# Kernel optimization log

Measured on AMD Instinct MI355X. Metric: run time of the kernel, lower is better.

The kernel has to match this reference:

```python
import jax, jax.numpy as jnp
import numpy as np

T, B, I, H = 2048, 64, 256, 256

def setup_inputs() -> dict:
    key = jax.random.key(0)
    k_x, k_wih, k_whh = jax.random.split(key, 3)
    x = jax.random.normal(k_x, (T, B, I), dtype=jnp.float32)
    h0 = jnp.zeros((1, B, H), dtype=jnp.float32)
    # nn.RNN weight_ih_l0 init: U(-1/sqrt(H), 1/sqrt(H)); shape [H, I]
    bound = 1.0 / np.sqrt(H)
    W_ih = jax.random.uniform(k_wih, (H, I), minval=-bound, maxval=bound, dtype=jnp.float32)
    # IndRNN recurrent weight: diagonal vector, U(-1, 1); biases are zeroed.
    w_hh = jax.random.uniform(k_whh, (H,), minval=-1.0, maxval=1.0, dtype=jnp.float32)
    return {"x": x, "h0": h0, "W_ih": W_ih, "w_hh": w_hh}

def reference(x, h0, W_ih, w_hh):
    # Precompute the input projection for all timesteps (the only GEMM):
    # [T, B, H] = x @ W_ih^T  (biases are zero)
    xW = jnp.einsum('tbi,hi->tbh', x, W_ih)

    def step(h, xw_t):
        # IndRNN: diagonal recurrence -> elementwise multiply instead of matmul
        h_new = jax.nn.relu(xw_t + h * w_hh)
        return h_new, h_new

    h_last, outputs = jax.lax.scan(step, h0[0], xW)
    return outputs, h_last[None]  # ([T,B,H], [1,B,H]) matching nn.RNN
```

## Files before the change

### kernel.cpp

```cpp
#include <hip/hip_runtime.h>

typedef short v8s __attribute__((ext_vector_type(8)));
typedef float v4f __attribute__((ext_vector_type(4)));

#define BATCH 16
#define NBATCH 128
#define BH 16384
#define TBH 33554432

__device__ __forceinline__ ushort f2bf(float f) {
  uint u = __float_as_uint(f);
  u += 0x7FFF + ((u >> 16) & 1);
  return (ushort)(u >> 16);
}

__device__ __forceinline__ uint pkbf2(float a, float b) {
  uint r;
  asm("v_cvt_pk_bf16_f32 %0, %1, %2" : "=v"(r) : "v"(a), "v"(b));
  return r;
}

union frag_u { uint u[4]; v8s s; };

__global__ __launch_bounds__(256, 2) void indrnn_gemm(
    const float* __restrict__ A,
    const float* __restrict__ W,
    ushort* __restrict__ C)
{
  const int tid  = threadIdx.x;
  const int lane = tid & 63;
  const int wv   = tid >> 6;
  const int l15  = lane & 15;
  const int lhi  = lane >> 4;
  const int c0   = wv * 64;
  const int rowblk = blockIdx.x * 256;

  frag_u wfr[4][8];
  #pragma unroll
  for (int nt = 0; nt < 4; ++nt) {
    const float* pw = W + (((size_t)(c0 + nt * 16 + l15)) << 8) + (lhi << 3);
    #pragma unroll
    for (int kk = 0; kk < 8; ++kk) {
      const float4 w0 = *(const float4*)(pw + kk * 32);
      const float4 w1 = *(const float4*)(pw + kk * 32 + 4);
      wfr[nt][kk].u[0] = pkbf2(w0.x, w0.y);
      wfr[nt][kk].u[1] = pkbf2(w0.z, w0.w);
      wfr[nt][kk].u[2] = pkbf2(w1.x, w1.y);
      wfr[nt][kk].u[3] = pkbf2(w1.z, w1.w);
    }
  }

  const float* pA = A + (((size_t)(rowblk + l15)) << 8) + (lhi << 3);

  float4 fa[8], fb[8];
  #pragma unroll
  for (int kk = 0; kk < 4; ++kk) {
    fa[2*kk]   = *(const float4*)(pA + kk * 32);
    fa[2*kk+1] = *(const float4*)(pA + kk * 32 + 4);
    fb[2*kk]   = *(const float4*)(pA + 128 + kk * 32);
    fb[2*kk+1] = *(const float4*)(pA + 128 + kk * 32 + 4);
  }

  for (int c = 0; c < 16; ++c) {
    v4f acc[4] = {};
    const float* pAn = pA + (size_t)(c + 1) * 4096;

    #pragma unroll
    for (int kk = 0; kk < 4; ++kk) {
      frag_u af;
      af.u[0] = pkbf2(fa[2*kk].x,   fa[2*kk].y);
      af.u[1] = pkbf2(fa[2*kk].z,   fa[2*kk].w);
      af.u[2] = pkbf2(fa[2*kk+1].x, fa[2*kk+1].y);
      af.u[3] = pkbf2(fa[2*kk+1].z, fa[2*kk+1].w);
      #pragma unroll
      for (int nt = 0; nt < 4; ++nt)
        acc[nt] = __builtin_amdgcn_mfma_f32_16x16x32_bf16(af.s, wfr[nt][kk].s, acc[nt], 0, 0, 0);
    }
    if (c + 1 < 16) {
      #pragma unroll
      for (int kk = 0; kk < 4; ++kk) {
        fa[2*kk]   = *(const float4*)(pAn + kk * 32);
        fa[2*kk+1] = *(const float4*)(pAn + kk * 32 + 4);
      }
    }

    #pragma unroll
    for (int kk = 0; kk < 4; ++kk) {
      frag_u af;
      af.u[0] = pkbf2(fb[2*kk].x,   fb[2*kk].y);
      af.u[1] = pkbf2(fb[2*kk].z,   fb[2*kk].w);
      af.u[2] = pkbf2(fb[2*kk+1].x, fb[2*kk+1].y);
      af.u[3] = pkbf2(fb[2*kk+1].z, fb[2*kk+1].w);
      #pragma unroll
      for (int nt = 0; nt < 4; ++nt)
        acc[nt] = __builtin_amdgcn_mfma_f32_16x16x32_bf16(af.s, wfr[nt][kk + 4].s, acc[nt], 0, 0, 0);
    }
    if (c + 1 < 16) {
      #pragma unroll
      for (int kk = 0; kk < 4; ++kk) {
        fb[2*kk]   = *(const float4*)(pAn + 128 + kk * 32);
        fb[2*kk+1] = *(const float4*)(pAn + 128 + kk * 32 + 4);
      }
    }

    const int mrow = rowblk + c * 16 + lhi * 4;
    #pragma unroll
    for (int nt = 0; nt < 4; ++nt) {
      const int col = c0 + nt * 16 + l15;
      #pragma unroll
      for (int r = 0; r < 4; ++r)
        C[(((size_t)(mrow + r)) << 8) + col] = f2bf(acc[nt][r]);
    }
  }
}

__global__ __launch_bounds__(64) void indrnn_scan(
    const ushort* __restrict__ xw,
    const float* __restrict__ h0,
    const float* __restrict__ w_hh,
    float* __restrict__ out)
{
  const int ch = blockIdx.x * 64 + threadIdx.x;
  const float w = w_hh[ch & 255];
  float h = h0[ch];
  const ushort* px = xw + ch;
  float* po = out + ch;

  uint b0[BATCH], b1[BATCH], b2[BATCH], b3[BATCH];

  auto ld = [&](uint (&buf)[BATCH], int kb) {
    const ushort* p = px + (size_t)kb * BATCH * BH;
    #pragma unroll
    for (int j = 0; j < BATCH; ++j) buf[j] = p[(size_t)j * BH];
  };
  auto cp = [&](uint (&buf)[BATCH], int kb) {
    float* o = po + (size_t)kb * BATCH * BH;
    #pragma unroll
    for (int j = 0; j < BATCH; ++j) {
      float xv = __uint_as_float(buf[j] << 16);
      h = fmaxf(fmaf(h, w, xv), 0.0f);
      o[(size_t)j * BH] = h;
    }
  };

  ld(b0, 0); ld(b1, 1); ld(b2, 2); ld(b3, 3);
  for (int kb = 0; kb < NBATCH; kb += 4) {
    cp(b0, kb);     if (kb + 4 < NBATCH) ld(b0, kb + 4);
    cp(b1, kb + 1); if (kb + 5 < NBATCH) ld(b1, kb + 5);
    cp(b2, kb + 2); if (kb + 6 < NBATCH) ld(b2, kb + 6);
    cp(b3, kb + 3); if (kb + 7 < NBATCH) ld(b3, kb + 7);
  }
  out[(size_t)TBH + ch] = h;
}

extern "C" void kernel_launch(void* const* d_in, const int* in_sizes, int n_in,
                              void* d_out, int out_size, void* d_ws, size_t ws_size,
                              hipStream_t stream) {
  const float* x    = (const float*)d_in[0];
  const float* h0   = (const float*)d_in[1];
  const float* W_ih = (const float*)d_in[2];
  const float* w_hh = (const float*)d_in[3];
  float* out = (float*)d_out;
  ushort* xw = (ushort*)d_ws;

  indrnn_gemm<<<dim3(512), dim3(256), 0, stream>>>(x, W_ih, xw);
  indrnn_scan<<<dim3(256), dim3(64), 0, stream>>>(xw, h0, w_hh, out);
}
```

Before: 321.1 us.

## Stage GEMM A tiles in LDS with async global_load_lds double buffering

In the input-projection GEMM, each wave used to load its own copy of the activation rows into registers. Now each 16-row A tile is loaded once per block, straight into a double-buffered, XOR-swizzled shared-memory buffer with global_load_lds, and every wave reads its fragments from LDS. The next tile's load overlaps the current tile's MFMAs, blocks are halved to 128 rows, the grid doubles and launch bounds ask for 4 blocks per CU. In exchange it adds 32 KB of LDS per block and a __syncthreads per tile, and the wait for the async loads to land relies on the barrier placement.

```diff
diff --git a/kernel.cpp b/kernel.cpp
--- a/kernel.cpp
+++ b/kernel.cpp
@@ -22,18 +22,30 @@
 
 union frag_u { uint u[4]; v8s s; };
 
-__global__ __launch_bounds__(256, 2) void indrnn_gemm(
+__global__ __launch_bounds__(256, 4) void indrnn_gemm(
     const float* __restrict__ A,
     const float* __restrict__ W,
     ushort* __restrict__ C)
 {
+  __shared__ __align__(16) float sbuf[2][4096];
+
   const int tid  = threadIdx.x;
   const int lane = tid & 63;
   const int wv   = tid >> 6;
   const int l15  = lane & 15;
   const int lhi  = lane >> 4;
   const int c0   = wv * 64;
-  const int rowblk = blockIdx.x * 256;
+  const int m0   = blockIdx.x * 128;
+
+  {
+    const float* base = A + ((size_t)m0 << 8);
+    #pragma unroll
+    for (int j = 0; j < 4; ++j) {
+      const int row = wv * 4 + j;
+      const float* src = base + (row << 8) + ((lane ^ (row & 7)) << 2);
+      __builtin_amdgcn_global_load_lds(src, &sbuf[0][row << 8], 16, 0, 0);
+    }
+  }
 
   frag_u wfr[4][8];
   #pragma unroll
@@ -50,60 +62,43 @@
     }
   }
 
-  const float* pA = A + (((size_t)(rowblk + l15)) << 8) + (lhi << 3);
+  const int swm  = (l15 & 7) << 4;
+  const int off0 = (l15 << 10) + ((lhi * 32)      ^ swm);
+  const int off1 = (l15 << 10) + ((lhi * 32 + 16) ^ swm);
 
-  float4 fa[8], fb[8];
-  #pragma unroll
-  for (int kk = 0; kk < 4; ++kk) {
-    fa[2*kk]   = *(const float4*)(pA + kk * 32);
-    fa[2*kk+1] = *(const float4*)(pA + kk * 32 + 4);
-    fb[2*kk]   = *(const float4*)(pA + 128 + kk * 32);
-    fb[2*kk+1] = *(const float4*)(pA + 128 + kk * 32 + 4);
-  }
+  __syncthreads();
 
-  for (int c = 0; c < 16; ++c) {
+  for (int c = 0; c < 8; ++c) {
+    const int cur = c & 1;
+
+    if (c + 1 < 8) {
+      const float* base = A + (((size_t)(m0 + (c + 1) * 16)) << 8);
+      #pragma unroll
+      for (int j = 0; j < 4; ++j) {
+        const int row = wv * 4 + j;
+        const float* src = base + (row << 8) + ((lane ^ (row & 7)) << 2);
+        __builtin_amdgcn_global_load_lds(src, &sbuf[cur ^ 1][row << 8], 16, 0, 0);
+      }
+    }
+
+    const char* p0 = (const char*)sbuf[cur] + off0;
+    const char* p1 = (const char*)sbuf[cur] + off1;
     v4f acc[4] = {};
-    const float* pAn = pA + (size_t)(c + 1) * 4096;
-
     #pragma unroll
-    for (int kk = 0; kk < 4; ++kk) {
+    for (int kk = 0; kk < 8; ++kk) {
+      const float4 f0 = *(const float4*)(p0 + kk * 128);
+      const float4 f1 = *(const float4*)(p1 + kk * 128);
       frag_u af;
-      af.u[0] = pkbf2(fa[2*kk].x,   fa[2*kk].y);
-      af.u[1] = pkbf2(fa[2*kk].z,   fa[2*kk].w);
-      af.u[2] = pkbf2(fa[2*kk+1].x, fa[2*kk+1].y);
-      af.u[3] = pkbf2(fa[2*kk+1].z, fa[2*kk+1].w);
+      af.u[0] = pkbf2(f0.x, f0.y);
+      af.u[1] = pkbf2(f0.z, f0.w);
+      af.u[2] = pkbf2(f1.x, f1.y);
+      af.u[3] = pkbf2(f1.z, f1.w);
       #pragma unroll
       for (int nt = 0; nt < 4; ++nt)
         acc[nt] = __builtin_amdgcn_mfma_f32_16x16x32_bf16(af.s, wfr[nt][kk].s, acc[nt], 0, 0, 0);
     }
-    if (c + 1 < 16) {
-      #pragma unroll
-      for (int kk = 0; kk < 4; ++kk) {
-        fa[2*kk]   = *(const float4*)(pAn + kk * 32);
-        fa[2*kk+1] = *(const float4*)(pAn + kk * 32 + 4);
-      }
-    }
 
-    #pragma unroll
-    for (int kk = 0; kk < 4; ++kk) {
-      frag_u af;
-      af.u[0] = pkbf2(fb[2*kk].x,   fb[2*kk].y);
-      af.u[1] = pkbf2(fb[2*kk].z,   fb[2*kk].w);
-      af.u[2] = pkbf2(fb[2*kk+1].x, fb[2*kk+1].y);
-      af.u[3] = pkbf2(fb[2*kk+1].z, fb[2*kk+1].w);
-      #pragma unroll
-      for (int nt = 0; nt < 4; ++nt)
-        acc[nt] = __builtin_amdgcn_mfma_f32_16x16x32_bf16(af.s, wfr[nt][kk + 4].s, acc[nt], 0, 0, 0);
-    }
-    if (c + 1 < 16) {
-      #pragma unroll
-      for (int kk = 0; kk < 4; ++kk) {
-        fb[2*kk]   = *(const float4*)(pAn + 128 + kk * 32);
-        fb[2*kk+1] = *(const float4*)(pAn + 128 + kk * 32 + 4);
-      }
-    }
-
-    const int mrow = rowblk + c * 16 + lhi * 4;
+    const int mrow = m0 + c * 16 + lhi * 4;
     #pragma unroll
     for (int nt = 0; nt < 4; ++nt) {
       const int col = c0 + nt * 16 + l15;
@@ -111,6 +106,8 @@
       for (int r = 0; r < 4; ++r)
         C[(((size_t)(mrow + r)) << 8) + col] = f2bf(acc[nt][r]);
     }
+
+    __syncthreads();
   }
 }
 
@@ -163,6 +160,6 @@
   float* out = (float*)d_out;
   ushort* xw = (ushort*)d_ws;
 
-  indrnn_gemm<<<dim3(512), dim3(256), 0, stream>>>(x, W_ih, xw);
+  indrnn_gemm<<<dim3(1024), dim3(256), 0, stream>>>(x, W_ih, xw);
   indrnn_scan<<<dim3(256), dim3(64), 0, stream>>>(xw, h0, w_hh, out);
 }
```

Result: slower. 362.9 us (+13.0%).
